# Optimization experiments

Hardware: AMD Instinct MI355X
Metric: run time of the kernel (lower is better)

Reference implementation:

```python
import jax, jax.numpy as jnp
import numpy as np

BASE_THETA = 0.5
K_DOP = 0.2
K_NOR = 0.15
K_SERO = 0.1
DIM = 1024


def setup_inputs() -> dict:
    key = jax.random.key(0)
    ks = jax.random.split(key, 9)
    scale = 1.0 / np.sqrt(DIM)
    x = jax.random.normal(ks[0], (2, 2048, DIM), dtype=jnp.float32)
    Wq = jax.random.normal(ks[1], (DIM, DIM), dtype=jnp.float32) * scale
    bq = jnp.zeros((DIM,), dtype=jnp.float32)
    Wk = jax.random.normal(ks[2], (DIM, DIM), dtype=jnp.float32) * scale
    bk = jnp.zeros((DIM,), dtype=jnp.float32)
    Wv = jax.random.normal(ks[3], (DIM, DIM), dtype=jnp.float32) * scale
    bv = jnp.zeros((DIM,), dtype=jnp.float32)
    Wo = jax.random.normal(ks[4], (DIM, DIM), dtype=jnp.float32) * scale
    bo = jnp.zeros((DIM,), dtype=jnp.float32)
    return {"x": x, "Wq": Wq, "bq": bq, "Wk": Wk, "bk": bk,
            "Wv": Wv, "bv": bv, "Wo": Wo, "bo": bo}


def reference(x, Wq, bq, Wk, bk, Wv, bv, Wo, bo):
    # Projections: torch nn.Linear computes x @ W.T + b
    q = jnp.einsum('bsd,ed->bse', x, Wq) + bq
    k = jnp.einsum('bsd,ed->bse', x, Wk) + bk
    v = jnp.einsum('bsd,ed->bse', x, Wv) + bv
    # Full [B, S, S] scores (no 1/sqrt(d) scaling in the original)
    qk = jnp.einsum('bsd,btd->bst', q, k)
    theta = (BASE_THETA
             + K_DOP * jax.nn.sigmoid(qk)
             + K_NOR * jnp.tanh(qk)
             + K_SERO * jax.nn.relu(qk))
    attn = jax.nn.softmax(theta, axis=-1)
    out = jnp.einsum('bst,btd->bsd', attn, v)
    return jnp.einsum('bsd,ed->bse', out, Wo) + bo
```

## Files before the change

kernel.cpp:

```cpp
#include <hip/hip_runtime.h>
#include <hip/hip_fp16.h>
#include <stdint.h>

typedef _Float16 f16;
typedef __attribute__((ext_vector_type(8))) _Float16 f16x8;
typedef __attribute__((ext_vector_type(4))) _Float16 f16x4;
typedef __attribute__((ext_vector_type(4))) float f32x4;

#define SEQ 2048
#define DIM 1024
#define NBATCH 2
#define MTOT 4096

__global__ void fill_kernel(float* p, float v, int n){
  int i = blockIdx.x * 256 + threadIdx.x;
  if (i < n) p[i] = v;
}

__global__ void cvt_all(const float* __restrict__ x, const float* __restrict__ Wq,
                        const float* __restrict__ Wk, const float* __restrict__ Wv,
                        const float* __restrict__ Wo,
                        f16* __restrict__ x16, f16* __restrict__ Wcat, f16* __restrict__ Wo16,
                        float* __restrict__ rowacc){
  int b = blockIdx.x;
  if (b == 8192){
    float4 z = {0.f, 0.f, 0.f, 0.f};
#pragma unroll
    for (int i = 0; i < 4; i++) ((float4*)rowacc)[threadIdx.x + i * 256] = z;
    return;
  }
  const float* src; f16* dst; int i;
  if (b < 4096){
    src = x; dst = x16; i = b * 256 + threadIdx.x;
  } else {
    int t = (b - 4096) >> 10;
    i = ((b - 4096) & 1023) * 256 + threadIdx.x;
    src = t == 0 ? Wq : t == 1 ? Wk : t == 2 ? Wv : Wo;
    dst = (t == 3) ? Wo16 : Wcat + (size_t)t * DIM * DIM;
  }
  float4 v = ((const float4*)src)[i];
  ((f16x4*)dst)[i] = (f16x4){(f16)v.x, (f16)v.y, (f16)v.z, (f16)v.w};
}

#define GLOAD16(SRC, DST) __builtin_amdgcn_global_load_lds( \
    (__attribute__((address_space(1))) void*)(SRC), \
    (__attribute__((address_space(3))) void*)(DST), 16, 0, 0)

__device__ __forceinline__ float theta_exp(float v){
  const float e1 = __expf(-v);
  const float sg = 1.f / (1.f + e1);
  const float e2 = e1 * e1;
  const float th = 2.f / (1.f + e2) - 1.f;
  const float theta = 0.5f + 0.2f * sg + 0.15f * th + 0.1f * fmaxf(v, 0.f);
  return __expf(fminf(theta - 10.f, 11.f));
}

__global__ __launch_bounds__(256, 3)
void gemm_qkv(const f16* __restrict__ A0, const f16* __restrict__ B0,
              f16* __restrict__ O0, f16* __restrict__ O1,
              const float* __restrict__ c0, const float* __restrict__ c1,
              const float* __restrict__ c2)
{
  __shared__ __align__(16) f16 As[8192];
  __shared__ __align__(16) f16 Bs[8192];
  const int tid  = threadIdx.x;
  const int lane = tid & 63;
  const int wid  = tid >> 6;
  const int bm = blockIdx.x, bn = blockIdx.y;

  const int s_r  = tid >> 3;
  const int s_cb = (tid & 7) ^ (s_r & 7);
  const f16* Ab = A0 + (long)(bm * 128 + s_r) * DIM + s_cb * 8;
  const f16* Bb = B0 + (long)(bn * 128 + s_r) * DIM + s_cb * 8;

  const int l15 = lane & 15, l7 = lane & 7, lhi = lane >> 4;
  const int wrow = (wid >> 1) * 64;
  const int wcol = (wid & 1) * 64;
  const int ar = (wrow + l15) * 64;
  const int br = (wcol + l15) * 64;
  const int cb0 = ((0 + lhi) ^ l7) * 8;
  const int cb1 = ((4 + lhi) ^ l7) * 8;

  f32x4 acc[4][4] = {};

  for (int t = 0; t < 16; ++t){
    __syncthreads();
    GLOAD16(Ab + (long)t*64,                  &As[       tid*8]);
    GLOAD16(Ab + (long)t*64 + (long)32 * DIM, &As[2048 + tid*8]);
    GLOAD16(Ab + (long)t*64 + (long)64 * DIM, &As[4096 + tid*8]);
    GLOAD16(Ab + (long)t*64 + (long)96 * DIM, &As[6144 + tid*8]);
    GLOAD16(Bb + (long)t*64,                  &Bs[       tid*8]);
    GLOAD16(Bb + (long)t*64 + (long)32 * DIM, &Bs[2048 + tid*8]);
    GLOAD16(Bb + (long)t*64 + (long)64 * DIM, &Bs[4096 + tid*8]);
    GLOAD16(Bb + (long)t*64 + (long)96 * DIM, &Bs[6144 + tid*8]);
    __syncthreads();
    f16x8 af[4], bf[4];
#pragma unroll
    for (int i = 0; i < 4; i++) af[i] = *(const f16x8*)&As[ar + i * 1024 + cb0];
#pragma unroll
    for (int j = 0; j < 4; j++) bf[j] = *(const f16x8*)&Bs[br + j * 1024 + cb0];
#pragma unroll
    for (int i = 0; i < 4; i++)
#pragma unroll
      for (int j = 0; j < 4; j++)
        acc[i][j] = __builtin_amdgcn_mfma_f32_16x16x32_f16(af[i], bf[j], acc[i][j], 0, 0, 0);
#pragma unroll
    for (int i = 0; i < 4; i++) af[i] = *(const f16x8*)&As[ar + i * 1024 + cb1];
#pragma unroll
    for (int j = 0; j < 4; j++) bf[j] = *(const f16x8*)&Bs[br + j * 1024 + cb1];
#pragma unroll
    for (int i = 0; i < 4; i++)
#pragma unroll
      for (int j = 0; j < 4; j++)
        acc[i][j] = __builtin_amdgcn_mfma_f32_16x16x32_f16(af[i], bf[j], acc[i][j], 0, 0, 0);
  }

  const int cc = l15;
  const int rr = lhi * 4;
#pragma unroll
  for (int i = 0; i < 4; i++)
#pragma unroll
    for (int j = 0; j < 4; j++){
      const int col = bn * 128 + wcol + j * 16 + cc;
      if (col < 2048){
        const float badd = (col < 1024) ? c0[col] : c1[col - 1024];
#pragma unroll
        for (int r = 0; r < 4; r++){
          const int row = bm * 128 + wrow + i * 16 + rr + r;
          O0[(long)row * 2048 + col] = (f16)(acc[i][j][r] + badd);
        }
      } else {
        const int dcol = col - 2048;
        const float badd = c2[dcol];
#pragma unroll
        for (int r = 0; r < 4; r++){
          const int row = bm * 128 + wrow + i * 16 + rr + r;
          O1[(long)row * DIM + dcol] = (f16)(acc[i][j][r] + badd);
        }
      }
    }
}

__global__ __launch_bounds__(256, 5)
void gemm_merged(const f16* __restrict__ qkcat, const f16* __restrict__ vbuf,
                 const f16* __restrict__ Wo16,
                 f16* __restrict__ Pbuf, f16* __restrict__ vWoT,
                 float* __restrict__ rowacc)
{
  __shared__ __align__(16) f16 As[8192];
  __shared__ __align__(16) f16 Bs[8192];
  const int tid  = threadIdx.x;
  const int lane = tid & 63;
  const int wid  = tid >> 6;
  const int l15 = lane & 15, l7 = lane & 7, lhi = lane >> 4;
  const int s_r  = tid >> 3;
  const int s_cb = (tid & 7) ^ (s_r & 7);
  const int cb0 = ((0 + lhi) ^ l7) * 8;
  const int cb1 = ((4 + lhi) ^ l7) * 8;
  const int cc = l15, rr = lhi * 4;
  const int r = blockIdx.x;

  if (r < 1024){
    const int bz = r >> 9, q = r & 511, bm = q >> 5, bn = q & 31;
    const f16* Ag = qkcat + (long)bz * SEQ * 2048;
    const f16* Bg = qkcat + DIM + (long)bz * SEQ * 2048;
    const f16* Ab = Ag + (long)(bm * 128 + s_r) * 2048 + s_cb * 8;
    const f16* Bb = Bg + (long)(bn * 64  + s_r) * 2048 + s_cb * 8;

    const int wrow = (wid >> 1) * 64;
    const int wcol = (wid & 1) * 32;
    const int ar = (wrow + l15) * 64;
    const int br = (wcol + l15) * 64;

    f32x4 acc[4][2] = {};

    for (int t = 0; t < 16; ++t){
      __syncthreads();
      GLOAD16(Ab + (long)t*64,                   &As[       tid*8]);
      GLOAD16(Ab + (long)t*64 + (long)32 * 2048, &As[2048 + tid*8]);
      GLOAD16(Ab + (long)t*64 + (long)64 * 2048, &As[4096 + tid*8]);
      GLOAD16(Ab + (long)t*64 + (long)96 * 2048, &As[6144 + tid*8]);
      GLOAD16(Bb + (long)t*64,                   &Bs[       tid*8]);
      GLOAD16(Bb + (long)t*64 + (long)32 * 2048, &Bs[2048 + tid*8]);
      __syncthreads();
      f16x8 af[4], bf[2];
#pragma unroll
      for (int i = 0; i < 4; i++) af[i] = *(const f16x8*)&As[ar + i * 1024 + cb0];
#pragma unroll
      for (int j = 0; j < 2; j++) bf[j] = *(const f16x8*)&Bs[br + j * 1024 + cb0];
#pragma unroll
      for (int i = 0; i < 4; i++)
#pragma unroll
        for (int j = 0; j < 2; j++)
          acc[i][j] = __builtin_amdgcn_mfma_f32_16x16x32_f16(af[i], bf[j], acc[i][j], 0, 0, 0);
#pragma unroll
      for (int i = 0; i < 4; i++) af[i] = *(const f16x8*)&As[ar + i * 1024 + cb1];
#pragma unroll
      for (int j = 0; j < 2; j++) bf[j] = *(const f16x8*)&Bs[br + j * 1024 + cb1];
#pragma unroll
      for (int i = 0; i < 4; i++)
#pragma unroll
        for (int j = 0; j < 2; j++)
          acc[i][j] = __builtin_amdgcn_mfma_f32_16x16x32_f16(af[i], bf[j], acc[i][j], 0, 0, 0);
    }

#pragma unroll
    for (int i = 0; i < 4; i++)
#pragma unroll
      for (int rq = 0; rq < 4; rq++){
        const int row = bm * 128 + wrow + i * 16 + rr + rq;
        float rs = 0.f;
#pragma unroll
        for (int j = 0; j < 2; j++){
          const int col = bn * 64 + wcol + j * 16 + cc;
          const float P = theta_exp(acc[i][j][rq]);
          Pbuf[(long)bz * SEQ * SEQ + (long)row * SEQ + col] = (f16)P;
          rs += P;
        }
        rs += __shfl_xor(rs, 1, 64);
        rs += __shfl_xor(rs, 2, 64);
        rs += __shfl_xor(rs, 4, 64);
        rs += __shfl_xor(rs, 8, 64);
        if (cc == 0) atomicAdd(&rowacc[bz * SEQ + row], rs);
      }
  } else {
    const int q = r - 1024;
    const int bz = q >> 7, qq = q & 127, bm = qq & 15, bn = qq >> 4;
    const f16* Ag = vbuf + (long)bz * SEQ * DIM;
    const f16* Ab = Ag + (long)(bm * 128 + s_r) * DIM + s_cb * 8;
    const f16* Bb = Wo16 + (long)(bn * 128 + s_r) * DIM + s_cb * 8;

    const int wrow = (wid >> 1) * 64;
    const int wcol = (wid & 1) * 64;
    const int ar = (wrow + l15) * 64;
    const int br = (wcol + l15) * 64;

    f32x4 acc[4][4] = {};

    for (int t = 0; t < 16; ++t){
      __syncthreads();
      GLOAD16(Ab + (long)t*64,                  &As[       tid*8]);
      GLOAD16(Ab + (long)t*64 + (long)32 * DIM, &As[2048 + tid*8]);
      GLOAD16(Ab + (long)t*64 + (long)64 * DIM, &As[4096 + tid*8]);
      GLOAD16(Ab + (long)t*64 + (long)96 * DIM, &As[6144 + tid*8]);
      GLOAD16(Bb + (long)t*64,                  &Bs[       tid*8]);
      GLOAD16(Bb + (long)t*64 + (long)32 * DIM, &Bs[2048 + tid*8]);
      GLOAD16(Bb + (long)t*64 + (long)64 * DIM, &Bs[4096 + tid*8]);
      GLOAD16(Bb + (long)t*64 + (long)96 * DIM, &Bs[6144 + tid*8]);
      __syncthreads();
      f16x8 af[4], bf[4];
#pragma unroll
      for (int i = 0; i < 4; i++) af[i] = *(const f16x8*)&As[ar + i * 1024 + cb0];
#pragma unroll
      for (int j = 0; j < 4; j++) bf[j] = *(const f16x8*)&Bs[br + j * 1024 + cb0];
#pragma unroll
      for (int i = 0; i < 4; i++)
#pragma unroll
        for (int j = 0; j < 4; j++)
          acc[i][j] = __builtin_amdgcn_mfma_f32_16x16x32_f16(af[i], bf[j], acc[i][j], 0, 0, 0);
#pragma unroll
      for (int i = 0; i < 4; i++) af[i] = *(const f16x8*)&As[ar + i * 1024 + cb1];
#pragma unroll
      for (int j = 0; j < 4; j++) bf[j] = *(const f16x8*)&Bs[br + j * 1024 + cb1];
#pragma unroll
      for (int i = 0; i < 4; i++)
#pragma unroll
        for (int j = 0; j < 4; j++)
          acc[i][j] = __builtin_amdgcn_mfma_f32_16x16x32_f16(af[i], bf[j], acc[i][j], 0, 0, 0);
    }

#pragma unroll
    for (int i = 0; i < 4; i++)
#pragma unroll
      for (int j = 0; j < 4; j++){
        const int col = bn * 128 + wcol + j * 16 + cc;
        const int row0 = bm * 128 + wrow + i * 16 + rr;
        f16x4 pk = {(f16)acc[i][j][0], (f16)acc[i][j][1],
                    (f16)acc[i][j][2], (f16)acc[i][j][3]};
        *(f16x4*)&vWoT[(long)bz * DIM * SEQ + (long)col * SEQ + row0] = pk;
      }
  }
}

__global__ __launch_bounds__(256, 4)
void gemm_final(const f16* __restrict__ Pb, const f16* __restrict__ Vw,
                float* __restrict__ psum)
{
  __shared__ __align__(16) f16 As[8192];
  __shared__ __align__(16) f16 Bs[8192];
  const int tid  = threadIdx.x;
  const int lane = tid & 63;
  const int wid  = tid >> 6;
  const int bm = blockIdx.x, bn = blockIdx.y;
  const int bz = blockIdx.z >> 1, kh = blockIdx.z & 1;

  const f16* Ag = Pb + (long)bz * SEQ * SEQ + (long)kh * 1024;
  const f16* Bg = Vw + (long)bz * DIM * SEQ + (long)kh * 1024;

  const int s_r  = tid >> 3;
  const int s_cb = (tid & 7) ^ (s_r & 7);
  const f16* Ab = Ag + (long)(bm * 128 + s_r) * 2048 + s_cb * 8;
  const f16* Bb = Bg + (long)(bn * 128 + s_r) * 2048 + s_cb * 8;

  const int l15 = lane & 15, l7 = lane & 7, lhi = lane >> 4;
  const int wrow = (wid >> 1) * 64;
  const int wcol = (wid & 1) * 64;
  const int ar = (wrow + l15) * 64;
  const int br = (wcol + l15) * 64;
  const int cb0 = ((0 + lhi) ^ l7) * 8;
  const int cb1 = ((4 + lhi) ^ l7) * 8;

  f32x4 acc[4][4] = {};

  for (int t = 0; t < 16; ++t){
    __syncthreads();
    GLOAD16(Ab + (long)t*64,                   &As[       tid*8]);
    GLOAD16(Ab + (long)t*64 + (long)32 * 2048, &As[2048 + tid*8]);
    GLOAD16(Ab + (long)t*64 + (long)64 * 2048, &As[4096 + tid*8]);
    GLOAD16(Ab + (long)t*64 + (long)96 * 2048, &As[6144 + tid*8]);
    GLOAD16(Bb + (long)t*64,                   &Bs[       tid*8]);
    GLOAD16(Bb + (long)t*64 + (long)32 * 2048, &Bs[2048 + tid*8]);
    GLOAD16(Bb + (long)t*64 + (long)64 * 2048, &Bs[4096 + tid*8]);
    GLOAD16(Bb + (long)t*64 + (long)96 * 2048, &Bs[6144 + tid*8]);
    __syncthreads();
    f16x8 af[4], bf[4];
#pragma unroll
    for (int i = 0; i < 4; i++) af[i] = *(const f16x8*)&As[ar + i * 1024 + cb0];
#pragma unroll
    for (int j = 0; j < 4; j++) bf[j] = *(const f16x8*)&Bs[br + j * 1024 + cb0];
#pragma unroll
    for (int i = 0; i < 4; i++)
#pragma unroll
      for (int j = 0; j < 4; j++)
        acc[i][j] = __builtin_amdgcn_mfma_f32_16x16x32_f16(af[i], bf[j], acc[i][j], 0, 0, 0);
#pragma unroll
    for (int i = 0; i < 4; i++) af[i] = *(const f16x8*)&As[ar + i * 1024 + cb1];
#pragma unroll
    for (int j = 0; j < 4; j++) bf[j] = *(const f16x8*)&Bs[br + j * 1024 + cb1];
#pragma unroll
    for (int i = 0; i < 4; i++)
#pragma unroll
      for (int j = 0; j < 4; j++)
        acc[i][j] = __builtin_amdgcn_mfma_f32_16x16x32_f16(af[i], bf[j], acc[i][j], 0, 0, 0);
  }

  const int cc = l15;
  const int rr = lhi * 4;
  float* Po = psum + (long)kh * MTOT * DIM + (long)bz * SEQ * DIM;
#pragma unroll
  for (int i = 0; i < 4; i++)
#pragma unroll
    for (int j = 0; j < 4; j++){
      const int col = bn * 128 + wcol + j * 16 + cc;
#pragma unroll
      for (int r = 0; r < 4; r++){
        const int row = bm * 128 + wrow + i * 16 + rr + r;
        Po[(long)row * DIM + col] = acc[i][j][r];
      }
    }
}

__global__ __launch_bounds__(256)
void combine_kernel(const float* __restrict__ psum, const float* __restrict__ rowacc,
                    const float* __restrict__ bo, float* __restrict__ out)
{
  const long i = (long)blockIdx.x * 256 + threadIdx.x;
  const int row = (int)(i >> 8);
  const int c4  = (int)(i & 255);
  float4 a = ((const float4*)psum)[i];
  float4 b = ((const float4*)(psum + (size_t)MTOT * DIM))[i];
  float4 bb = ((const float4*)bo)[c4];
  const float inv = 1.f / rowacc[row];
  float4 o;
  o.x = (a.x + b.x) * inv + bb.x;
  o.y = (a.y + b.y) * inv + bb.y;
  o.z = (a.z + b.z) * inv + bb.z;
  o.w = (a.w + b.w) * inv + bb.w;
  ((float4*)out)[i] = o;
}

extern "C" void kernel_launch(void* const* d_in, const int* in_sizes, int n_in,
                              void* d_out, int out_size, void* d_ws, size_t ws_size,
                              hipStream_t stream){
  const float* x  = (const float*)d_in[0];
  const float* Wq = (const float*)d_in[1];
  const float* bq = (const float*)d_in[2];
  const float* Wk = (const float*)d_in[3];
  const float* bk = (const float*)d_in[4];
  const float* Wv = (const float*)d_in[5];
  const float* bv = (const float*)d_in[6];
  const float* Wo = (const float*)d_in[7];
  const float* bo = (const float*)d_in[8];
  float* out = (float*)d_out;

  char* ws = (char*)d_ws;
  size_t off = 0;
  auto alloc = [&](size_t bytes) -> char* {
    char* p = ws + off; off += (bytes + 255) & ~(size_t)255; return p;
  };

  f16* x16     = (f16*)alloc(2ull * MTOT * DIM);
  f16* Wcat    = (f16*)alloc(2ull * 3 * DIM * DIM);
  f16* Wo16    = (f16*)alloc(2ull * DIM * DIM);
  f16* qkcat   = (f16*)alloc(2ull * MTOT * 2 * DIM);
  f16* vbuf    = (f16*)alloc(2ull * MTOT * DIM);
  f16* Pbuf    = (f16*)alloc(2ull * NBATCH * SEQ * SEQ);
  f16* vWoT    = (f16*)alloc(2ull * NBATCH * DIM * SEQ);
  float* rowac = (float*)alloc(4ull * MTOT);
  float* psum  = (float*)alloc(4ull * 2 * MTOT * DIM);

  if (off > ws_size){
    fill_kernel<<<(out_size + 255) / 256, 256, 0, stream>>>(out, 12345.0f, out_size);
    return;
  }

  cvt_all<<<8193, 256, 0, stream>>>(x, Wq, Wk, Wv, Wo, x16, Wcat, Wo16, rowac);

  gemm_qkv<<<dim3(MTOT / 128, 3 * DIM / 128, 1), 256, 0, stream>>>(
      x16, Wcat, qkcat, vbuf, bq, bk, bv);

  gemm_merged<<<1280, 256, 0, stream>>>(qkcat, vbuf, Wo16, Pbuf, vWoT, rowac);

  gemm_final<<<dim3(SEQ / 128, DIM / 128, 2 * NBATCH), 256, 0, stream>>>(
      Pbuf, vWoT, psum);

  combine_kernel<<<MTOT * DIM / 4 / 256, 256, 0, stream>>>(psum, rowac, bo, out);
}
```

Measured before the change: 128.9 us.

## Fuse split-K combine into final GEMM via atomics, enlarge QK tiles, remap blocks

```diff
diff --git a/kernel.cpp b/kernel.cpp
--- a/kernel.cpp
+++ b/kernel.cpp
@@ -19,10 +19,15 @@
 
 __global__ void cvt_all(const float* __restrict__ x, const float* __restrict__ Wq,
                         const float* __restrict__ Wk, const float* __restrict__ Wv,
-                        const float* __restrict__ Wo,
+                        const float* __restrict__ Wo, const float* __restrict__ bo,
                         f16* __restrict__ x16, f16* __restrict__ Wcat, f16* __restrict__ Wo16,
-                        float* __restrict__ rowacc){
+                        float* __restrict__ rowacc, float* __restrict__ out){
   int b = blockIdx.x;
+  if (b >= 8193){
+    const long i = (long)(b - 8193) * 256 + threadIdx.x;
+    ((float4*)out)[i] = ((const float4*)bo)[i & 255];
+    return;
+  }
   if (b == 8192){
     float4 z = {0.f, 0.f, 0.f, 0.f};
 #pragma unroll
@@ -83,6 +88,7 @@
 
   f32x4 acc[4][4] = {};
 
+#pragma unroll
   for (int t = 0; t < 16; ++t){
     __syncthreads();
     GLOAD16(Ab + (long)t*64,                  &As[       tid*8]);
@@ -141,7 +147,7 @@
     }
 }
 
-__global__ __launch_bounds__(256, 5)
+__global__ __launch_bounds__(256, 3)
 void gemm_merged(const f16* __restrict__ qkcat, const f16* __restrict__ vbuf,
                  const f16* __restrict__ Wo16,
                  f16* __restrict__ Pbuf, f16* __restrict__ vWoT,
@@ -158,22 +164,23 @@
   const int cb0 = ((0 + lhi) ^ l7) * 8;
   const int cb1 = ((4 + lhi) ^ l7) * 8;
   const int cc = l15, rr = lhi * 4;
+  const int wrow = (wid >> 1) * 64;
+  const int wcol = (wid & 1) * 64;
+  const int ar = (wrow + l15) * 64;
+  const int br = (wcol + l15) * 64;
   const int r = blockIdx.x;
 
-  if (r < 1024){
-    const int bz = r >> 9, q = r & 511, bm = q >> 5, bn = q & 31;
-    const f16* Ag = qkcat + (long)bz * SEQ * 2048;
-    const f16* Bg = qkcat + DIM + (long)bz * SEQ * 2048;
-    const f16* Ab = Ag + (long)(bm * 128 + s_r) * 2048 + s_cb * 8;
-    const f16* Bb = Bg + (long)(bn * 64  + s_r) * 2048 + s_cb * 8;
-
-    const int wrow = (wid >> 1) * 64;
-    const int wcol = (wid & 1) * 32;
-    const int ar = (wrow + l15) * 64;
-    const int br = (wcol + l15) * 64;
-
-    f32x4 acc[4][2] = {};
-
+  if (r < 512){
+    const int x = r & 7, i5 = r >> 3;
+    const int bz = x >> 2;
+    const int bn = (x & 3) * 4 + (i5 & 3);
+    const int bm = i5 >> 2;
+    const f16* Ab = qkcat + (long)bz * SEQ * 2048 + (long)(bm * 128 + s_r) * 2048 + s_cb * 8;
+    const f16* Bb = qkcat + DIM + (long)bz * SEQ * 2048 + (long)(bn * 128 + s_r) * 2048 + s_cb * 8;
+
+    f32x4 acc[4][4] = {};
+
+#pragma unroll
     for (int t = 0; t < 16; ++t){
       __syncthreads();
       GLOAD16(Ab + (long)t*64,                   &As[       tid*8]);
@@ -182,25 +189,27 @@
       GLOAD16(Ab + (long)t*64 + (long)96 * 2048, &As[6144 + tid*8]);
       GLOAD16(Bb + (long)t*64,                   &Bs[       tid*8]);
       GLOAD16(Bb + (long)t*64 + (long)32 * 2048, &Bs[2048 + tid*8]);
+      GLOAD16(Bb + (long)t*64 + (long)64 * 2048, &Bs[4096 + tid*8]);
+      GLOAD16(Bb + (long)t*64 + (long)96 * 2048, &Bs[6144 + tid*8]);
       __syncthreads();
-      f16x8 af[4], bf[2];
+      f16x8 af[4], bf[4];
 #pragma unroll
       for (int i = 0; i < 4; i++) af[i] = *(const f16x8*)&As[ar + i * 1024 + cb0];
 #pragma unroll
-      for (int j = 0; j < 2; j++) bf[j] = *(const f16x8*)&Bs[br + j * 1024 + cb0];
+      for (int j = 0; j < 4; j++) bf[j] = *(const f16x8*)&Bs[br + j * 1024 + cb0];
 #pragma unroll
       for (int i = 0; i < 4; i++)
 #pragma unroll
-        for (int j = 0; j < 2; j++)
+        for (int j = 0; j < 4; j++)
           acc[i][j] = __builtin_amdgcn_mfma_f32_16x16x32_f16(af[i], bf[j], acc[i][j], 0, 0, 0);
 #pragma unroll
       for (int i = 0; i < 4; i++) af[i] = *(const f16x8*)&As[ar + i * 1024 + cb1];
 #pragma unroll
-      for (int j = 0; j < 2; j++) bf[j] = *(const f16x8*)&Bs[br + j * 1024 + cb1];
+      for (int j = 0; j < 4; j++) bf[j] = *(const f16x8*)&Bs[br + j * 1024 + cb1];
 #pragma unroll
       for (int i = 0; i < 4; i++)
 #pragma unroll
-        for (int j = 0; j < 2; j++)
+        for (int j = 0; j < 4; j++)
           acc[i][j] = __builtin_amdgcn_mfma_f32_16x16x32_f16(af[i], bf[j], acc[i][j], 0, 0, 0);
     }
 
@@ -211,8 +220,8 @@
         const int row = bm * 128 + wrow + i * 16 + rr + rq;
         float rs = 0.f;
 #pragma unroll
-        for (int j = 0; j < 2; j++){
-          const int col = bn * 64 + wcol + j * 16 + cc;
+        for (int j = 0; j < 4; j++){
+          const int col = bn * 128 + wcol + j * 16 + cc;
           const float P = theta_exp(acc[i][j][rq]);
           Pbuf[(long)bz * SEQ * SEQ + (long)row * SEQ + col] = (f16)P;
           rs += P;
@@ -224,19 +233,17 @@
         if (cc == 0) atomicAdd(&rowacc[bz * SEQ + row], rs);
       }
   } else {
-    const int q = r - 1024;
-    const int bz = q >> 7, qq = q & 127, bm = qq & 15, bn = qq >> 4;
-    const f16* Ag = vbuf + (long)bz * SEQ * DIM;
-    const f16* Ab = Ag + (long)(bm * 128 + s_r) * DIM + s_cb * 8;
+    const int rr2 = r - 512;
+    const int x = rr2 & 7, i5 = rr2 >> 3;
+    const int bz = x >> 2;
+    const int bn = (x & 3) * 2 + (i5 & 1);
+    const int bm = i5 >> 1;
+    const f16* Ab = vbuf + (long)bz * SEQ * DIM + (long)(bm * 128 + s_r) * DIM + s_cb * 8;
     const f16* Bb = Wo16 + (long)(bn * 128 + s_r) * DIM + s_cb * 8;
 
-    const int wrow = (wid >> 1) * 64;
-    const int wcol = (wid & 1) * 64;
-    const int ar = (wrow + l15) * 64;
-    const int br = (wcol + l15) * 64;
-
     f32x4 acc[4][4] = {};
 
+#pragma unroll
     for (int t = 0; t < 16; ++t){
       __syncthreads();
       GLOAD16(Ab + (long)t*64,                  &As[       tid*8]);
@@ -282,17 +289,21 @@
   }
 }
 
-__global__ __launch_bounds__(256, 4)
+__global__ __launch_bounds__(256, 2)
 void gemm_final(const f16* __restrict__ Pb, const f16* __restrict__ Vw,
-                float* __restrict__ psum)
+                float* __restrict__ out, const float* __restrict__ rowacc)
 {
   __shared__ __align__(16) f16 As[8192];
   __shared__ __align__(16) f16 Bs[8192];
   const int tid  = threadIdx.x;
   const int lane = tid & 63;
   const int wid  = tid >> 6;
-  const int bm = blockIdx.x, bn = blockIdx.y;
-  const int bz = blockIdx.z >> 1, kh = blockIdx.z & 1;
+  const int r = blockIdx.x;
+  const int x = r & 7, i5 = r >> 3;
+  const int z4 = x >> 1;
+  const int bz = z4 >> 1, kh = z4 & 1;
+  const int bn = (x & 1) * 4 + (i5 & 3);
+  const int bm = i5 >> 2;
 
   const f16* Ag = Pb + (long)bz * SEQ * SEQ + (long)kh * 1024;
   const f16* Bg = Vw + (long)bz * DIM * SEQ + (long)kh * 1024;
@@ -312,6 +323,7 @@
 
   f32x4 acc[4][4] = {};
 
+#pragma unroll
   for (int t = 0; t < 16; ++t){
     __syncthreads();
     GLOAD16(Ab + (long)t*64,                   &As[       tid*8]);
@@ -346,37 +358,19 @@
 
   const int cc = l15;
   const int rr = lhi * 4;
-  float* Po = psum + (long)kh * MTOT * DIM + (long)bz * SEQ * DIM;
+  float* Ob = out + (long)bz * SEQ * DIM;
 #pragma unroll
   for (int i = 0; i < 4; i++)
 #pragma unroll
-    for (int j = 0; j < 4; j++){
-      const int col = bn * 128 + wcol + j * 16 + cc;
-#pragma unroll
-      for (int r = 0; r < 4; r++){
-        const int row = bm * 128 + wrow + i * 16 + rr + r;
-        Po[(long)row * DIM + col] = acc[i][j][r];
+    for (int r4 = 0; r4 < 4; r4++){
+      const int row = bm * 128 + wrow + i * 16 + rr + r4;
+      const float inv = 1.f / rowacc[bz * SEQ + row];
+#pragma unroll
+      for (int j = 0; j < 4; j++){
+        const int col = bn * 128 + wcol + j * 16 + cc;
+        atomicAdd(&Ob[(long)row * DIM + col], acc[i][j][r4] * inv);
       }
     }
-}
-
-__global__ __launch_bounds__(256)
-void combine_kernel(const float* __restrict__ psum, const float* __restrict__ rowacc,
-                    const float* __restrict__ bo, float* __restrict__ out)
-{
-  const long i = (long)blockIdx.x * 256 + threadIdx.x;
-  const int row = (int)(i >> 8);
-  const int c4  = (int)(i & 255);
-  float4 a = ((const float4*)psum)[i];
-  float4 b = ((const float4*)(psum + (size_t)MTOT * DIM))[i];
-  float4 bb = ((const float4*)bo)[c4];
-  const float inv = 1.f / rowacc[row];
-  float4 o;
-  o.x = (a.x + b.x) * inv + bb.x;
-  o.y = (a.y + b.y) * inv + bb.y;
-  o.z = (a.z + b.z) * inv + bb.z;
-  o.w = (a.w + b.w) * inv + bb.w;
-  ((float4*)out)[i] = o;
 }
 
 extern "C" void kernel_launch(void* const* d_in, const int* in_sizes, int n_in,
@@ -407,22 +401,19 @@
   f16* Pbuf    = (f16*)alloc(2ull * NBATCH * SEQ * SEQ);
   f16* vWoT    = (f16*)alloc(2ull * NBATCH * DIM * SEQ);
   float* rowac = (float*)alloc(4ull * MTOT);
-  float* psum  = (float*)alloc(4ull * 2 * MTOT * DIM);
 
   if (off > ws_size){
     fill_kernel<<<(out_size + 255) / 256, 256, 0, stream>>>(out, 12345.0f, out_size);
     return;
   }
 
-  cvt_all<<<8193, 256, 0, stream>>>(x, Wq, Wk, Wv, Wo, x16, Wcat, Wo16, rowac);
+  cvt_all<<<12289, 256, 0, stream>>>(x, Wq, Wk, Wv, Wo, bo,
+                                     x16, Wcat, Wo16, rowac, out);
 
   gemm_qkv<<<dim3(MTOT / 128, 3 * DIM / 128, 1), 256, 0, stream>>>(
       x16, Wcat, qkcat, vbuf, bq, bk, bv);
 
-  gemm_merged<<<1280, 256, 0, stream>>>(qkcat, vbuf, Wo16, Pbuf, vWoT, rowac);
-
-  gemm_final<<<dim3(SEQ / 128, DIM / 128, 2 * NBATCH), 256, 0, stream>>>(
-      Pbuf, vWoT, psum);
-
-  combine_kernel<<<MTOT * DIM / 4 / 256, 256, 0, stream>>>(psum, rowac, bo, out);
-}
+  gemm_merged<<<768, 256, 0, stream>>>(qkcat, vbuf, Wo16, Pbuf, vWoT, rowac);
+
+  gemm_final<<<512, 256, 0, stream>>>(Pbuf, vWoT, out, rowac);
+}
```

New measurement: 127.7 us. No clear change (-0.9%).
